# Kernel optimization log

Hardware: AMD Instinct MI355X
Metric: run time of the kernel (lower is better)

## Reference

```python
import jax, jax.numpy as jnp
import numpy as np

N_HARMONIC = 6
CONCAT = (3,)  # cfg.append_distance: concat embedding after this layer index
N_LAYERS = 8


def harmonic_embedding(x):
    # x: [N, 3] -> [N, 6*2*3 + 3] = [N, 39]
    freqs = 2.0 ** jnp.arange(N_HARMONIC, dtype=x.dtype)  # omega0 = 1.0, logspace
    embed = (x[..., None] * freqs).reshape(*x.shape[:-1], -1)  # [N, 18]
    return jnp.concatenate([jnp.sin(embed), jnp.cos(embed), x], axis=-1)


def setup_inputs() -> dict:
    key = jax.random.key(0)
    N, H, E = 262144, 256, 39
    ks = jax.random.split(key, 11)
    inp = {"points": jax.random.normal(ks[0], (N, 3), dtype=jnp.float32)}
    in_dims = [E, H, H, H, E + H, H, H, H]  # skip-concat before layer 4
    for i, d_in in enumerate(in_dims):
        scale = 1.0 / np.sqrt(d_in)
        inp[f"w{i}"] = jax.random.normal(ks[i + 1], (d_in, H), dtype=jnp.float32) * scale
        inp[f"b{i}"] = jnp.zeros((H,), dtype=jnp.float32)
    inp["wsdf"] = jax.random.normal(ks[9], (H, 1), dtype=jnp.float32) * (1.0 / np.sqrt(H))
    inp["bsdf"] = jnp.zeros((1,), dtype=jnp.float32)
    return inp


def reference(points, w0, b0, w1, b1, w2, b2, w3, b3, w4, b4, w5, b5, w6, b6, w7, b7, wsdf, bsdf):
    ws = [w0, w1, w2, w3, w4, w5, w6, w7]
    bs = [b0, b1, b2, b3, b4, b5, b6, b7]
    emb = harmonic_embedding(points.reshape(-1, 3))  # [N, 39]
    x = emb
    for i in range(N_LAYERS):
        x = jax.nn.relu(x @ ws[i] + bs[i])
        if i in CONCAT:
            x = jnp.concatenate([emb, x], axis=-1)  # torch.cat([add, xyz])
    return x @ wsdf + bsdf  # [N, 1] signed distance
```

## Files before the change

### kernel.cpp

```cpp
#include <hip/hip_runtime.h>
#include <hip/hip_fp16.h>

typedef _Float16 f16x8 __attribute__((ext_vector_type(8)));
typedef _Float16 f16x4 __attribute__((ext_vector_type(4)));
typedef float    f32x16 __attribute__((ext_vector_type(16)));
typedef float    f32x4 __attribute__((ext_vector_type(4)));

#define SH 264
#define SE 48
#define PTS 128

struct LayerPtrs {
  const float* w[8];
  const float* b[8];
};

__global__ void prep_weights(LayerPtrs P, f16x8* __restrict__ wf) {
  int gid = blockIdx.x * 256 + threadIdx.x;
  if (gid >= 60416) return;
  const int OFF[9] = {0,1536,9728,17920,26112,35840,44032,52224,60416};
  int l = 0;
  while (gid >= OFF[l+1]) ++l;
  int f = gid - OFF[l];
  int lane = f & 63;
  int t = f >> 6;
  int mtile = t & 7;
  int kc = t >> 3;
  int col = mtile * 32 + (lane & 31);
  int kb  = (lane >> 5) * 8;
  const float* w = P.w[l];
  f16x8 v;
#pragma unroll
  for (int j = 0; j < 8; ++j) {
    float x = 0.f;
    if (l == 4) {
      if (kc < 3) {
        int k = kc * 16 + kb + j;
        if (k < 39) x = w[k * 256 + col];
      } else {
        int k = (kc - 3) * 16 + kb + j;
        x = w[(39 + k) * 256 + col];
      }
    } else if (l == 0) {
      int k = kc * 16 + kb + j;
      if (k < 39) x = w[k * 256 + col];
    } else {
      int k = kc * 16 + kb + j;
      x = w[k * 256 + col];
    }
    v[j] = (_Float16)x;
  }
  wf[gid] = v;
}

template<int NKC, int STRIDE>
__device__ __forceinline__ void mm(const f16x8* __restrict__ wb,
                                   const _Float16* __restrict__ b0,
                                   const _Float16* __restrict__ b1,
                                   const _Float16* __restrict__ b2,
                                   const _Float16* __restrict__ b3,
                                   f32x16 acc[2][4]) {
#pragma unroll
  for (int kc = 0; kc < NKC; ++kc) {
    f16x8 a0 = wb[(kc * 8 + 0) * 64];
    f16x8 a1 = wb[(kc * 8 + 1) * 64];
    f16x8 v0 = *(const f16x8*)(b0 + kc * 16);
    f16x8 v1 = *(const f16x8*)(b1 + kc * 16);
    f16x8 v2 = *(const f16x8*)(b2 + kc * 16);
    f16x8 v3 = *(const f16x8*)(b3 + kc * 16);
    acc[0][0] = __builtin_amdgcn_mfma_f32_32x32x16_f16(a0, v0, acc[0][0], 0, 0, 0);
    acc[0][1] = __builtin_amdgcn_mfma_f32_32x32x16_f16(a0, v1, acc[0][1], 0, 0, 0);
    acc[0][2] = __builtin_amdgcn_mfma_f32_32x32x16_f16(a0, v2, acc[0][2], 0, 0, 0);
    acc[0][3] = __builtin_amdgcn_mfma_f32_32x32x16_f16(a0, v3, acc[0][3], 0, 0, 0);
    acc[1][0] = __builtin_amdgcn_mfma_f32_32x32x16_f16(a1, v0, acc[1][0], 0, 0, 0);
    acc[1][1] = __builtin_amdgcn_mfma_f32_32x32x16_f16(a1, v1, acc[1][1], 0, 0, 0);
    acc[1][2] = __builtin_amdgcn_mfma_f32_32x32x16_f16(a1, v2, acc[1][2], 0, 0, 0);
    acc[1][3] = __builtin_amdgcn_mfma_f32_32x32x16_f16(a1, v3, acc[1][3], 0, 0, 0);
  }
}

__device__ __forceinline__ void zero_acc(f32x16 acc[2][4]) {
#pragma unroll
  for (int mt = 0; mt < 2; ++mt)
#pragma unroll
    for (int nt = 0; nt < 4; ++nt)
#pragma unroll
      for (int r = 0; r < 16; ++r) acc[mt][nt][r] = 0.f;
}

__device__ __forceinline__ void store_act(f32x16 acc[2][4], const float* __restrict__ bp,
                                          int wv, int lane, _Float16* __restrict__ H) {
  int p0 = lane & 31, h = lane >> 5;
#pragma unroll
  for (int mt = 0; mt < 2; ++mt) {
    int hb = wv * 64 + mt * 32 + 4 * h;
#pragma unroll
    for (int g = 0; g < 4; ++g) {
      f32x4 bv = *(const f32x4*)&bp[hb + 8 * g];
#pragma unroll
      for (int nt = 0; nt < 4; ++nt) {
        f16x4 o;
#pragma unroll
        for (int r = 0; r < 4; ++r) {
          float x = acc[mt][nt][4 * g + r] + bv[r];
          o[r] = (_Float16)fmaxf(x, 0.f);
        }
        *(f16x4*)&H[(nt * 32 + p0) * SH + hb + 8 * g] = o;
      }
    }
  }
}

__global__ __launch_bounds__(256, 2)
void mlp_fused(const float* __restrict__ points,
               LayerPtrs P,
               const f16x8* __restrict__ wf,
               const float* __restrict__ wsdf,
               const float* __restrict__ bsdf,
               float* __restrict__ out) {
  __shared__ __align__(16) _Float16 H[PTS * SH];
  __shared__ __align__(16) _Float16 E[PTS * SE];
  const int tid = threadIdx.x;
  const int blk = blockIdx.x;

  if (tid < PTS) {
    int p = blk * PTS + tid;
    float xyz[3] = {points[p * 3 + 0], points[p * 3 + 1], points[p * 3 + 2]};
    _Float16* row = &E[tid * SE];
#pragma unroll
    for (int c = 0; c < 3; ++c) {
      float fr = 1.f;
#pragma unroll
      for (int k = 0; k < 6; ++k) {
        float e = xyz[c] * fr;
        row[c * 6 + k]      = (_Float16)sinf(e);
        row[18 + c * 6 + k] = (_Float16)cosf(e);
        fr *= 2.f;
      }
      row[36 + c] = (_Float16)xyz[c];
    }
#pragma unroll
    for (int c = 39; c < SE; ++c) row[c] = (_Float16)0.f;
  }
  __syncthreads();

  const int lane = tid & 63;
  const int wv   = tid >> 6;
  const int p0   = lane & 31;
  const int h    = lane >> 5;

  const _Float16* e0 = &E[p0 * SE + h * 8];
  const _Float16* e1 = &E[(32 + p0) * SE + h * 8];
  const _Float16* e2 = &E[(64 + p0) * SE + h * 8];
  const _Float16* e3 = &E[(96 + p0) * SE + h * 8];
  const _Float16* h0 = &H[p0 * SH + h * 8];
  const _Float16* h1 = &H[(32 + p0) * SH + h * 8];
  const _Float16* h2 = &H[(64 + p0) * SH + h * 8];
  const _Float16* h3 = &H[(96 + p0) * SH + h * 8];
  const f16x8* wb = wf + wv * 128 + lane;

  const int WOFF[8] = {0,1536,9728,17920,26112,35840,44032,52224};

  f32x16 acc[2][4];

  zero_acc(acc);
  mm<3, SE>(wb + WOFF[0], e0, e1, e2, e3, acc);
  store_act(acc, P.b[0], wv, lane, H);
  __syncthreads();

#pragma unroll
  for (int l = 1; l < 4; ++l) {
    zero_acc(acc);
    mm<16, SH>(wb + WOFF[l], h0, h1, h2, h3, acc);
    __syncthreads();
    store_act(acc, P.b[l], wv, lane, H);
    __syncthreads();
  }

  zero_acc(acc);
  mm<3, SE>(wb + WOFF[4], e0, e1, e2, e3, acc);
  mm<16, SH>(wb + WOFF[4] + 3 * 512, h0, h1, h2, h3, acc);
  __syncthreads();
  store_act(acc, P.b[4], wv, lane, H);
  __syncthreads();

#pragma unroll
  for (int l = 5; l < 8; ++l) {
    zero_acc(acc);
    mm<16, SH>(wb + WOFF[l], h0, h1, h2, h3, acc);
    __syncthreads();
    store_act(acc, P.b[l], wv, lane, H);
    __syncthreads();
  }

  {
    const int p = tid >> 1, part = tid & 1;
    float a = 0.f;
    const _Float16* xr = &H[p * SH + part * 128];
#pragma unroll
    for (int j = 0; j < 16; ++j) {
      f16x8 hh = *(const f16x8*)&xr[j * 8];
      f32x4 wa = *(const f32x4*)&wsdf[part * 128 + j * 8];
      f32x4 wc = *(const f32x4*)&wsdf[part * 128 + j * 8 + 4];
      a += (float)hh[0] * wa[0] + (float)hh[1] * wa[1]
         + (float)hh[2] * wa[2] + (float)hh[3] * wa[3]
         + (float)hh[4] * wc[0] + (float)hh[5] * wc[1]
         + (float)hh[6] * wc[2] + (float)hh[7] * wc[3];
    }
    a += __shfl_down(a, 1);
    if (part == 0) out[blk * PTS + p] = a + bsdf[0];
  }
}

extern "C" void kernel_launch(void* const* d_in, const int* in_sizes, int n_in,
                              void* d_out, int out_size, void* d_ws, size_t ws_size,
                              hipStream_t stream) {
  const float* points = (const float*)d_in[0];
  LayerPtrs P;
  for (int i = 0; i < 8; ++i) {
    P.w[i] = (const float*)d_in[1 + 2 * i];
    P.b[i] = (const float*)d_in[2 + 2 * i];
  }
  const float* wsdf = (const float*)d_in[17];
  const float* bsdf = (const float*)d_in[18];
  f16x8* wf = (f16x8*)d_ws;

  int N = in_sizes[0] / 3;
  prep_weights<<<236, 256, 0, stream>>>(P, wf);
  mlp_fused<<<N / PTS, 256, 0, stream>>>(points, P, wf, wsdf, bsdf, (float*)d_out);
}
```

Measured before the change: 318.0 us.

## Double points per block and give each wave a 128x128 output tile

Blocks now process 256 points, and each of the 4 waves computes a 128-feature by 128-point tile (4x4 MFMA tiles) instead of 64x128. Each weight fragment is reused across more points and each activation load feeds more MFMAs, cutting global weight traffic per point. The bias is folded into the accumulator initialisation rather than added at store time. In exchange the accumulator count doubles to 256 fp32 registers per lane, occupancy drops to one block per CU, and LDS use per block roughly doubles.

After: 372.2 us. 1.17x slower.

```diff
diff --git a/kernel.cpp b/kernel.cpp
--- a/kernel.cpp
+++ b/kernel.cpp
@@ -8,7 +8,7 @@
 
 #define SH 264
 #define SE 48
-#define PTS 128
+#define PTS 256
 
 struct LayerPtrs {
   const float* w[8];
@@ -53,17 +53,19 @@
   wf[gid] = v;
 }
 
-template<int NKC, int STRIDE>
+template<int NKC>
 __device__ __forceinline__ void mm(const f16x8* __restrict__ wb,
                                    const _Float16* __restrict__ b0,
                                    const _Float16* __restrict__ b1,
                                    const _Float16* __restrict__ b2,
                                    const _Float16* __restrict__ b3,
-                                   f32x16 acc[2][4]) {
+                                   f32x16 acc[4][4]) {
 #pragma unroll
   for (int kc = 0; kc < NKC; ++kc) {
     f16x8 a0 = wb[(kc * 8 + 0) * 64];
     f16x8 a1 = wb[(kc * 8 + 1) * 64];
+    f16x8 a2 = wb[(kc * 8 + 2) * 64];
+    f16x8 a3 = wb[(kc * 8 + 3) * 64];
     f16x8 v0 = *(const f16x8*)(b0 + kc * 16);
     f16x8 v1 = *(const f16x8*)(b1 + kc * 16);
     f16x8 v2 = *(const f16x8*)(b2 + kc * 16);
@@ -76,42 +78,53 @@
     acc[1][1] = __builtin_amdgcn_mfma_f32_32x32x16_f16(a1, v1, acc[1][1], 0, 0, 0);
     acc[1][2] = __builtin_amdgcn_mfma_f32_32x32x16_f16(a1, v2, acc[1][2], 0, 0, 0);
     acc[1][3] = __builtin_amdgcn_mfma_f32_32x32x16_f16(a1, v3, acc[1][3], 0, 0, 0);
-  }
-}
-
-__device__ __forceinline__ void zero_acc(f32x16 acc[2][4]) {
-#pragma unroll
-  for (int mt = 0; mt < 2; ++mt)
-#pragma unroll
-    for (int nt = 0; nt < 4; ++nt)
-#pragma unroll
-      for (int r = 0; r < 16; ++r) acc[mt][nt][r] = 0.f;
-}
-
-__device__ __forceinline__ void store_act(f32x16 acc[2][4], const float* __restrict__ bp,
-                                          int wv, int lane, _Float16* __restrict__ H) {
+    acc[2][0] = __builtin_amdgcn_mfma_f32_32x32x16_f16(a2, v0, acc[2][0], 0, 0, 0);
+    acc[2][1] = __builtin_amdgcn_mfma_f32_32x32x16_f16(a2, v1, acc[2][1], 0, 0, 0);
+    acc[2][2] = __builtin_amdgcn_mfma_f32_32x32x16_f16(a2, v2, acc[2][2], 0, 0, 0);
+    acc[2][3] = __builtin_amdgcn_mfma_f32_32x32x16_f16(a2, v3, acc[2][3], 0, 0, 0);
+    acc[3][0] = __builtin_amdgcn_mfma_f32_32x32x16_f16(a3, v0, acc[3][0], 0, 0, 0);
+    acc[3][1] = __builtin_amdgcn_mfma_f32_32x32x16_f16(a3, v1, acc[3][1], 0, 0, 0);
+    acc[3][2] = __builtin_amdgcn_mfma_f32_32x32x16_f16(a3, v2, acc[3][2], 0, 0, 0);
+    acc[3][3] = __builtin_amdgcn_mfma_f32_32x32x16_f16(a3, v3, acc[3][3], 0, 0, 0);
+  }
+}
+
+__device__ __forceinline__ void init_acc(f32x16 acc[4][4], const float* __restrict__ bp,
+                                         int h) {
+#pragma unroll
+  for (int mt = 0; mt < 4; ++mt)
+#pragma unroll
+    for (int g = 0; g < 4; ++g) {
+      f32x4 bv = *(const f32x4*)&bp[mt * 32 + 8 * g + 4 * h];
+#pragma unroll
+      for (int nt = 0; nt < 4; ++nt)
+#pragma unroll
+        for (int r = 0; r < 4; ++r)
+          acc[mt][nt][4 * g + r] = bv[r];
+    }
+}
+
+__device__ __forceinline__ void store_act(f32x16 acc[4][4], int wg, int pg,
+                                          int lane, _Float16* __restrict__ H) {
   int p0 = lane & 31, h = lane >> 5;
 #pragma unroll
-  for (int mt = 0; mt < 2; ++mt) {
-    int hb = wv * 64 + mt * 32 + 4 * h;
+  for (int mt = 0; mt < 4; ++mt) {
+    int hb = wg * 128 + mt * 32 + 4 * h;
 #pragma unroll
     for (int g = 0; g < 4; ++g) {
-      f32x4 bv = *(const f32x4*)&bp[hb + 8 * g];
 #pragma unroll
       for (int nt = 0; nt < 4; ++nt) {
         f16x4 o;
 #pragma unroll
-        for (int r = 0; r < 4; ++r) {
-          float x = acc[mt][nt][4 * g + r] + bv[r];
-          o[r] = (_Float16)fmaxf(x, 0.f);
-        }
-        *(f16x4*)&H[(nt * 32 + p0) * SH + hb + 8 * g] = o;
+        for (int r = 0; r < 4; ++r)
+          o[r] = (_Float16)fmaxf(acc[mt][nt][4 * g + r], 0.f);
+        *(f16x4*)&H[(pg * 128 + nt * 32 + p0) * SH + hb + 8 * g] = o;
       }
     }
   }
 }
 
-__global__ __launch_bounds__(256, 2)
+__global__ __launch_bounds__(256, 1)
 void mlp_fused(const float* __restrict__ points,
                LayerPtrs P,
                const f16x8* __restrict__ wf,
@@ -123,7 +136,7 @@
   const int tid = threadIdx.x;
   const int blk = blockIdx.x;
 
-  if (tid < PTS) {
+  {
     int p = blk * PTS + tid;
     float xyz[3] = {points[p * 3 + 0], points[p * 3 + 1], points[p * 3 + 2]};
     _Float16* row = &E[tid * SE];
@@ -146,69 +159,69 @@
 
   const int lane = tid & 63;
   const int wv   = tid >> 6;
+  const int wg   = wv & 1;
+  const int pg   = wv >> 1;
   const int p0   = lane & 31;
   const int h    = lane >> 5;
 
-  const _Float16* e0 = &E[p0 * SE + h * 8];
-  const _Float16* e1 = &E[(32 + p0) * SE + h * 8];
-  const _Float16* e2 = &E[(64 + p0) * SE + h * 8];
-  const _Float16* e3 = &E[(96 + p0) * SE + h * 8];
-  const _Float16* h0 = &H[p0 * SH + h * 8];
-  const _Float16* h1 = &H[(32 + p0) * SH + h * 8];
-  const _Float16* h2 = &H[(64 + p0) * SH + h * 8];
-  const _Float16* h3 = &H[(96 + p0) * SH + h * 8];
-  const f16x8* wb = wf + wv * 128 + lane;
+  const _Float16* e0 = &E[(pg * 128 +  0 + p0) * SE + h * 8];
+  const _Float16* e1 = &E[(pg * 128 + 32 + p0) * SE + h * 8];
+  const _Float16* e2 = &E[(pg * 128 + 64 + p0) * SE + h * 8];
+  const _Float16* e3 = &E[(pg * 128 + 96 + p0) * SE + h * 8];
+  const _Float16* h0 = &H[(pg * 128 +  0 + p0) * SH + h * 8];
+  const _Float16* h1 = &H[(pg * 128 + 32 + p0) * SH + h * 8];
+  const _Float16* h2 = &H[(pg * 128 + 64 + p0) * SH + h * 8];
+  const _Float16* h3 = &H[(pg * 128 + 96 + p0) * SH + h * 8];
+  const f16x8* wb = wf + (wg * 4) * 64 + lane;
 
   const int WOFF[8] = {0,1536,9728,17920,26112,35840,44032,52224};
 
-  f32x16 acc[2][4];
-
-  zero_acc(acc);
-  mm<3, SE>(wb + WOFF[0], e0, e1, e2, e3, acc);
-  store_act(acc, P.b[0], wv, lane, H);
+  f32x16 acc[4][4];
+
+  init_acc(acc, P.b[0] + wg * 128, h);
+  mm<3>(wb + WOFF[0], e0, e1, e2, e3, acc);
+  store_act(acc, wg, pg, lane, H);
   __syncthreads();
 
 #pragma unroll
   for (int l = 1; l < 4; ++l) {
-    zero_acc(acc);
-    mm<16, SH>(wb + WOFF[l], h0, h1, h2, h3, acc);
-    __syncthreads();
-    store_act(acc, P.b[l], wv, lane, H);
-    __syncthreads();
-  }
-
-  zero_acc(acc);
-  mm<3, SE>(wb + WOFF[4], e0, e1, e2, e3, acc);
-  mm<16, SH>(wb + WOFF[4] + 3 * 512, h0, h1, h2, h3, acc);
-  __syncthreads();
-  store_act(acc, P.b[4], wv, lane, H);
+    init_acc(acc, P.b[l] + wg * 128, h);
+    mm<16>(wb + WOFF[l], h0, h1, h2, h3, acc);
+    __syncthreads();
+    store_act(acc, wg, pg, lane, H);
+    __syncthreads();
+  }
+
+  init_acc(acc, P.b[4] + wg * 128, h);
+  mm<3>(wb + WOFF[4], e0, e1, e2, e3, acc);
+  mm<16>(wb + WOFF[4] + 3 * 512, h0, h1, h2, h3, acc);
+  __syncthreads();
+  store_act(acc, wg, pg, lane, H);
   __syncthreads();
 
 #pragma unroll
   for (int l = 5; l < 8; ++l) {
-    zero_acc(acc);
-    mm<16, SH>(wb + WOFF[l], h0, h1, h2, h3, acc);
-    __syncthreads();
-    store_act(acc, P.b[l], wv, lane, H);
+    init_acc(acc, P.b[l] + wg * 128, h);
+    mm<16>(wb + WOFF[l], h0, h1, h2, h3, acc);
+    __syncthreads();
+    store_act(acc, wg, pg, lane, H);
     __syncthreads();
   }
 
   {
-    const int p = tid >> 1, part = tid & 1;
     float a = 0.f;
-    const _Float16* xr = &H[p * SH + part * 128];
-#pragma unroll
-    for (int j = 0; j < 16; ++j) {
+    const _Float16* xr = &H[tid * SH];
+#pragma unroll
+    for (int j = 0; j < 32; ++j) {
       f16x8 hh = *(const f16x8*)&xr[j * 8];
-      f32x4 wa = *(const f32x4*)&wsdf[part * 128 + j * 8];
-      f32x4 wc = *(const f32x4*)&wsdf[part * 128 + j * 8 + 4];
+      f32x4 wa = *(const f32x4*)&wsdf[j * 8];
+      f32x4 wc = *(const f32x4*)&wsdf[j * 8 + 4];
       a += (float)hh[0] * wa[0] + (float)hh[1] * wa[1]
          + (float)hh[2] * wa[2] + (float)hh[3] * wa[3]
          + (float)hh[4] * wc[0] + (float)hh[5] * wc[1]
          + (float)hh[6] * wc[2] + (float)hh[7] * wc[3];
     }
-    a += __shfl_down(a, 1);
-    if (part == 0) out[blk * PTS + p] = a + bsdf[0];
+    out[blk * PTS + tid] = a + bsdf[0];
   }
 }
 
```
